# Kernel optimization log

Measured on AMD Instinct MI355X. Metric: run time of the kernel, lower is better.

Reference implementation:

```python
import jax, jax.numpy as jnp
import numpy as np
from jax import lax

EPS = 1e-5


def fps(xyz, npoint):
    # Farthest point sampling; xyz [B, N, 3] -> idx [B, npoint] (starts at point 0)
    B, N, _ = xyz.shape

    def body(carry, _):
        dist, far = carry
        c = jnp.take_along_axis(xyz, far[:, None, None], axis=1)  # [B,1,3]
        d = jnp.sum((xyz - c) ** 2, -1)                            # [B,N]
        dist = jnp.minimum(dist, d)
        nxt = jnp.argmax(dist, -1).astype(jnp.int32)
        return (dist, nxt), far

    init = (jnp.full((B, N), 1e10, xyz.dtype), jnp.zeros((B,), jnp.int32))
    _, idx = lax.scan(body, init, None, length=npoint)
    return idx.T  # [B, npoint]


def query_ball(radius, nsample, xyz, new_xyz):
    # xyz [B,N,3], new_xyz [B,S,3] -> idx [B,S,nsample]
    N = xyz.shape[1]
    sqr = jnp.sum((new_xyz[:, :, None, :] - xyz[:, None, :, :]) ** 2, -1)  # [B,S,N]
    idx = jnp.where(sqr > radius * radius, N, jnp.arange(N)[None, None, :])
    idx = jnp.sort(idx, axis=-1)[:, :, :nsample]
    # out-of-ball slots get replaced by the first in-ball index (torch repo behavior)
    return jnp.where(idx == N, idx[:, :, :1], idx)


def gather_pts(x, idx):
    # x [B,N,C], idx [B,...] -> [B,...,C]
    B = x.shape[0]
    b = jnp.arange(B).reshape((B,) + (1,) * (idx.ndim - 1))
    return x[b, idx]


def mlp_bn(x, layers):
    # x [B,S,K,C]; shared 1x1-conv MLP + training-mode BatchNorm + ReLU
    for w, g, b in layers:
        x = jnp.einsum('bskc,oc->bsko', x, w)
        mean = x.mean((0, 1, 2))
        var = x.var((0, 1, 2))  # biased, as torch BN uses for normalization
        x = jax.nn.relu((x - mean) * lax.rsqrt(var + EPS) * g + b)
    return x


def set_abstraction(xyz, points, npoint, radius, nsample, layers, group_all):
    B = xyz.shape[0]
    if group_all:
        new_xyz = jnp.zeros((B, 1, 3), xyz.dtype)
        new_points = xyz[:, None]  # [B,1,N,3] (raw xyz, no centering)
        if points is not None:
            new_points = jnp.concatenate([new_points, points[:, None]], -1)
    else:
        fidx = fps(xyz, npoint)
        new_xyz = gather_pts(xyz, fidx)                     # [B,S,3]
        idx = query_ball(radius, nsample, xyz, new_xyz)     # [B,S,K]
        grouped = gather_pts(xyz, idx) - new_xyz[:, :, None, :]
        if points is not None:
            new_points = jnp.concatenate([grouped, gather_pts(points, idx)], -1)
        else:
            new_points = grouped
    feat = mlp_bn(new_points, layers).max(2)  # max-pool over neighbors -> [B,S,C]
    return new_xyz, feat


def _forward(xyz_time, l1, l2, l3):
    B, T, N, _ = xyz_time.shape
    x = xyz_time.reshape(B * T, N, 4)
    xyz, t = x[..., :3], x[..., 3:]
    x1_xyz, x1 = set_abstraction(xyz, t, 512, 0.2, 32, l1, False)
    x2_xyz, x2 = set_abstraction(x1_xyz, x1, 128, 0.4, 64, l2, False)
    _, x3 = set_abstraction(x2_xyz, x2, None, None, None, l3, True)
    return x3.reshape(B, T, -1)


def setup_inputs() -> dict:
    key = jax.random.key(0)
    ks = jax.random.split(key, 16)
    inp = {"xyz_time": jax.random.uniform(ks[0], (2, 4, 4096, 4), jnp.float32)}
    specs = {1: [(64, 4), (64, 64), (128, 64)],
             2: [(128, 131), (128, 128), (256, 128)],
             3: [(256, 259), (512, 256), (1024, 512)]}
    i = 1
    for s, layers in specs.items():
        for j, (o, c) in enumerate(layers):
            inp[f"w{s}_{j}"] = jax.random.normal(jax.random.fold_in(ks[i], j), (o, c), jnp.float32) * 0.1
            inp[f"g{s}_{j}"] = jnp.ones((o,), jnp.float32)
            inp[f"b{s}_{j}"] = jnp.zeros((o,), jnp.float32)
        i += 1
    return inp


def reference(xyz_time, w1_0, g1_0, b1_0, w1_1, g1_1, b1_1, w1_2, g1_2, b1_2,
              w2_0, g2_0, b2_0, w2_1, g2_1, b2_1, w2_2, g2_2, b2_2,
              w3_0, g3_0, b3_0, w3_1, g3_1, b3_1, w3_2, g3_2, b3_2):
    l1 = [(w1_0, g1_0, b1_0), (w1_1, g1_1, b1_1), (w1_2, g1_2, b1_2)]
    l2 = [(w2_0, g2_0, b2_0), (w2_1, g2_1, b2_1), (w2_2, g2_2, b2_2)]
    l3 = [(w3_0, g3_0, b3_0), (w3_1, g3_1, b3_1), (w3_2, g3_2, b3_2)]
    return _forward(xyz_time, l1, l2, l3)
```

## Files before the change

kernel.cpp:

```cpp
#include <hip/hip_runtime.h>


typedef short s16x8 __attribute__((ext_vector_type(8)));
typedef float f32x4 __attribute__((ext_vector_type(4)));

__device__ __forceinline__ unsigned short f2bf_rne(float f) {
    unsigned u = __float_as_uint(f);
    u += 0x7FFFu + ((u >> 16) & 1u);
    return (unsigned short)(u >> 16);
}
__device__ __forceinline__ void f2bf_split(float v, unsigned short& hi,
                                           unsigned short& lo) {
    unsigned u = __float_as_uint(v);
    unsigned r = u + 0x7FFFu + ((u >> 16) & 1u);
    hi = (unsigned short)(r >> 16);
    float vh = __uint_as_float(r & 0xFFFF0000u);
    lo = f2bf_rne(v - vh);
}

__device__ __forceinline__ unsigned long long umax64(unsigned long long a,
                                                     unsigned long long b) {
    return a > b ? a : b;
}

__device__ __forceinline__ unsigned wred_umax63(unsigned v) {
    unsigned t;
    t = (unsigned)__builtin_amdgcn_update_dpp(0, (int)v, 0x111, 0xf, 0xf, true); if (t > v) v = t;
    t = (unsigned)__builtin_amdgcn_update_dpp(0, (int)v, 0x112, 0xf, 0xf, true); if (t > v) v = t;
    t = (unsigned)__builtin_amdgcn_update_dpp(0, (int)v, 0x114, 0xf, 0xf, true); if (t > v) v = t;
    t = (unsigned)__builtin_amdgcn_update_dpp(0, (int)v, 0x118, 0xf, 0xf, true); if (t > v) v = t;
    t = (unsigned)__builtin_amdgcn_update_dpp(0, (int)v, 0x142, 0xa, 0xf, true); if (t > v) v = t;
    t = (unsigned)__builtin_amdgcn_update_dpp(0, (int)v, 0x143, 0xc, 0xf, true); if (t > v) v = t;
    return v;
}

__device__ __forceinline__ void wave_argmax(unsigned dbits, unsigned nInv,
                                            unsigned& vmax, unsigned& iInv) {
    unsigned m = wred_umax63(dbits);
    vmax = (unsigned)__builtin_amdgcn_readlane((int)m, 63);
    unsigned cand = (dbits == vmax) ? nInv : 0u;
    unsigned im = wred_umax63(cand);
    iInv = (unsigned)__builtin_amdgcn_readlane((int)im, 63);
}

struct PWArgs {
    const float* w[9];
    unsigned off[9];
    int O[9], C[9], CP[9];
};
__device__ __forceinline__ void prep_w_dev(const PWArgs& a,
                                           unsigned short* __restrict__ wh,
                                           unsigned short* __restrict__ wl,
                                           int i) {
    int l = 0;
#pragma unroll
    for (int k = 1; k < 9; ++k) if (i >= (int)a.off[k]) l = k;
    int li = i - (int)a.off[l];
    int CP = a.CP[l];
    int o = li / CP;
    int c = li - o * CP;
    float v = (c < a.C[l]) ? a.w[l][(size_t)o * a.C[l] + c] : 0.f;
    unsigned short h, lo;
    f2bf_split(v, h, lo);
    wh[i] = h; wl[i] = lo;
}

template<int NT, int ITEMS, int STRIDE>
__global__ __launch_bounds__(NT) void fps_block(
    const float* __restrict__ pts, int npoint,
    int* __restrict__ outIdx, float* __restrict__ outXyz,
    int nFps, PWArgs pw, unsigned short* __restrict__ wh,
    unsigned short* __restrict__ wl, int wtotal)
{
    constexpr int N = NT * ITEMS;
    constexpr int NW = NT / 64;
    __shared__ float4 scoord[N];
    __shared__ unsigned long long wkey[2][NW];

    if (blockIdx.x >= nFps) {
        int i = (blockIdx.x - nFps) * NT + threadIdx.x;
        if (i < wtotal) prep_w_dev(pw, wh, wl, i);
        return;
    }

    const int b = blockIdx.x;
    const int tid = threadIdx.x;
    const int wid = tid >> 6;
    const int lane = tid & 63;
    const float* P = pts + (size_t)b * N * STRIDE;

    float px[ITEMS], py[ITEMS], pz[ITEMS], dloc[ITEMS];
#pragma unroll
    for (int w = 0; w < ITEMS; ++w) {
        int n = tid + w * NT;
        float x, y, z;
        if (STRIDE == 4) {
            float4 v = *(const float4*)(P + (size_t)n * 4);
            x = v.x; y = v.y; z = v.z;
        } else {
            x = P[(size_t)n * STRIDE + 0];
            y = P[(size_t)n * STRIDE + 1];
            z = P[(size_t)n * STRIDE + 2];
        }
        px[w] = x; py[w] = y; pz[w] = z;
        scoord[n] = make_float4(x, y, z, 0.f);
        dloc[w] = 1e10f;
    }
    __syncthreads();
    float4 c0 = scoord[0];
    float cx = c0.x, cy = c0.y, cz = c0.z;
    int far = 0;

    for (int i = 0; i < npoint; ++i) {
        if (tid == 0) {
            outIdx[(size_t)b * npoint + i] = far;
            outXyz[((size_t)b * npoint + i) * 3 + 0] = cx;
            outXyz[((size_t)b * npoint + i) * 3 + 1] = cy;
            outXyz[((size_t)b * npoint + i) * 3 + 2] = cz;
        }
        float bestV = -1.0f;
        int bestW = 0;
#pragma unroll
        for (int w = 0; w < ITEMS; ++w) {
            float dx = __fsub_rn(px[w], cx);
            float dy = __fsub_rn(py[w], cy);
            float dz = __fsub_rn(pz[w], cz);
            float d = __fadd_rn(__fadd_rn(__fmul_rn(dx, dx), __fmul_rn(dy, dy)),
                                __fmul_rn(dz, dz));
            float dd = fminf(dloc[w], d);
            dloc[w] = dd;
            if (dd > bestV) { bestV = dd; bestW = w; }
        }
        int bestN = tid + bestW * NT;
        unsigned vmax, iInv;
        wave_argmax(__float_as_uint(bestV), 0xFFFFFFFFu ^ (unsigned)bestN,
                    vmax, iInv);
        const int par = i & 1;
        if (lane == 0)
            wkey[par][wid] = ((unsigned long long)vmax << 32) | iInv;
        __syncthreads();
        unsigned long long kb = wkey[par][0];
#pragma unroll
        for (int w2 = 1; w2 < NW; ++w2) kb = umax64(kb, wkey[par][w2]);
        far = (int)(0xFFFFFFFFu ^ (unsigned)kb);
        float4 cc = scoord[far];
        cx = cc.x; cy = cc.y; cz = cc.z;
    }
}

__device__ void fps_wave_dev(const float* __restrict__ pts, int npoint,
                             int* __restrict__ outIdx, float* __restrict__ outXyz,
                             int b, float4* scoord)
{
    constexpr int ITEMS = 8;
    constexpr int STRIDE = 3;
    constexpr int N = 64 * ITEMS;
    const int tid = threadIdx.x;
    const float* P = pts + (size_t)b * N * STRIDE;

    float px[ITEMS], py[ITEMS], pz[ITEMS], dloc[ITEMS];
#pragma unroll
    for (int w = 0; w < ITEMS; ++w) {
        int n = tid + w * 64;
        float x = P[(size_t)n * STRIDE + 0];
        float y = P[(size_t)n * STRIDE + 1];
        float z = P[(size_t)n * STRIDE + 2];
        px[w] = x; py[w] = y; pz[w] = z;
        scoord[n] = make_float4(x, y, z, 0.f);
        dloc[w] = 1e10f;
    }
    __threadfence_block();
    float4 c0 = scoord[0];
    float cx = c0.x, cy = c0.y, cz = c0.z;
    int far = 0;

    for (int i = 0; i < npoint; ++i) {
        if (tid == 0) {
            outIdx[(size_t)b * npoint + i] = far;
            outXyz[((size_t)b * npoint + i) * 3 + 0] = cx;
            outXyz[((size_t)b * npoint + i) * 3 + 1] = cy;
            outXyz[((size_t)b * npoint + i) * 3 + 2] = cz;
        }
        float bestV = -1.0f;
        int bestW = 0;
#pragma unroll
        for (int w = 0; w < ITEMS; ++w) {
            float dx = __fsub_rn(px[w], cx);
            float dy = __fsub_rn(py[w], cy);
            float dz = __fsub_rn(pz[w], cz);
            float d = __fadd_rn(__fadd_rn(__fmul_rn(dx, dx), __fmul_rn(dy, dy)),
                                __fmul_rn(dz, dz));
            float dd = fminf(dloc[w], d);
            dloc[w] = dd;
            if (dd > bestV) { bestV = dd; bestW = w; }
        }
        int bestN = tid + bestW * 64;
        unsigned vmax, iInv;
        wave_argmax(__float_as_uint(bestV), 0xFFFFFFFFu ^ (unsigned)bestN,
                    vmax, iInv);
        far = (int)(0xFFFFFFFFu ^ iInv);
        float4 cc = scoord[far];
        cx = cc.x; cy = cc.y; cz = cc.z;
    }
}

__global__ __launch_bounds__(256) void qb_group1(
    const float* __restrict__ xyz ,
    const float* __restrict__ ctr ,
    float* __restrict__ out )
{
    int gw = (blockIdx.x * 256 + threadIdx.x) >> 6;
    int lane = threadIdx.x & 63;
    if (gw >= 4096) return;
    int b = gw >> 9;
    const float* P = xyz + (size_t)b * 4096 * 4;
    float cx = ctr[(size_t)gw * 3 + 0];
    float cy = ctr[(size_t)gw * 3 + 1];
    float cz = ctr[(size_t)gw * 3 + 2];
    float* out0 = out + (size_t)gw * 32 * 8;
    int cnt = 0;
    float f0x = 0.f, f0y = 0.f, f0z = 0.f, f0t = 0.f;
    bool haveFirst = false;
    for (int base = 0; base < 4096 && cnt < 32; base += 64) {
        int n = base + lane;
        float4 p = *(const float4*)(P + (size_t)n * 4);
        float ex = __fsub_rn(p.x, cx);
        float ey = __fsub_rn(p.y, cy);
        float ez = __fsub_rn(p.z, cz);
        float d = __fadd_rn(__fadd_rn(__fmul_rn(ex, ex), __fmul_rn(ey, ey)),
                            __fmul_rn(ez, ez));
        bool inb = !(d > 0.04f);
        unsigned long long mask = __ballot(inb);
        if (mask) {
            if (!haveFirst) {
                int fl = (int)__builtin_ctzll(mask);
                f0x = __shfl(ex, fl); f0y = __shfl(ey, fl);
                f0z = __shfl(ez, fl); f0t = __shfl(p.w, fl);
                haveFirst = true;
            }
            if (inb) {
                int pos = cnt + __builtin_popcountll(mask & ((1ull << lane) - 1ull));
                if (pos < 32) {
                    float* o = out0 + (size_t)pos * 8;
                    *(float4*)o = make_float4(ex, ey, ez, p.w);
                    *(float4*)(o + 4) = make_float4(0.f, 0.f, 0.f, 0.f);
                }
            }
            cnt += (int)__builtin_popcountll(mask);
        }
    }
    if (cnt > 32) cnt = 32;
    for (int p2 = cnt + lane; p2 < 32; p2 += 64) {
        float* o = out0 + (size_t)p2 * 8;
        *(float4*)o = make_float4(f0x, f0y, f0z, f0t);
        *(float4*)(o + 4) = make_float4(0.f, 0.f, 0.f, 0.f);
    }
}

__global__ __launch_bounds__(256) void query_ball_kernel(
    const float* __restrict__ xyz, int stride, int N,
    const float* __restrict__ centers, int nCenters, int S,
    float r2, int nsample, int* __restrict__ outIdx)
{
    int gw = (blockIdx.x * 256 + threadIdx.x) >> 6;
    int lane = threadIdx.x & 63;
    if (gw >= nCenters) return;
    int b = gw / S;
    const float* P = xyz + (size_t)b * N * stride;
    float cx = centers[(size_t)gw * 3 + 0];
    float cy = centers[(size_t)gw * 3 + 1];
    float cz = centers[(size_t)gw * 3 + 2];
    int* out = outIdx + (size_t)gw * nsample;
    int cnt = 0;
    int firstIdx = 0;
    bool haveFirst = false;
    for (int base = 0; base < N && cnt < nsample; base += 64) {
        int n = base + lane;
        bool inb = false;
        if (n < N) {
            float dx = __fsub_rn(cx, P[(size_t)n * stride + 0]);
            float dy = __fsub_rn(cy, P[(size_t)n * stride + 1]);
            float dz = __fsub_rn(cz, P[(size_t)n * stride + 2]);
            float d = __fadd_rn(__fadd_rn(__fmul_rn(dx, dx), __fmul_rn(dy, dy)),
                                __fmul_rn(dz, dz));
            inb = !(d > r2);
        }
        unsigned long long mask = __ballot(inb);
        if (mask) {
            if (!haveFirst) { firstIdx = base + __builtin_ctzll(mask); haveFirst = true; }
            if (inb) {
                int pos = cnt + __builtin_popcountll(mask & ((1ull << lane) - 1ull));
                if (pos < nsample) out[pos] = n;
            }
            cnt += (int)__builtin_popcountll(mask);
        }
    }
    if (cnt > nsample) cnt = nsample;
    for (int p = cnt + lane; p < nsample; p += 64) out[p] = firstIdx;
}

__global__ __launch_bounds__(256) void group2_kernel(
    const float* __restrict__ xyz, const float* __restrict__ feat,
    const int* __restrict__ qb, const float* __restrict__ ctr,
    float* __restrict__ out)
{
    int i = blockIdx.x * 256 + threadIdx.x;
    if (i >= 65536 * 136) return;
    int sk = i / 136;
    int c = i - sk * 136;
    int b = sk / (128 * 64);
    int bs = sk / 64;
    int idx = qb[sk];
    idx = (idx < 0) ? 0 : (idx > 511 ? 511 : idx);
    float v = 0.f;
    if (c < 3)        v = __fsub_rn(xyz[((size_t)b * 512 + idx) * 3 + c], ctr[(size_t)bs * 3 + c]);
    else if (c < 131) v = feat[((size_t)b * 512 + idx) * 128 + (c - 3)];
    out[i] = v;
}

__global__ __launch_bounds__(256) void group3_kernel(
    const float* __restrict__ ctr2, const float* __restrict__ feat2,
    float* __restrict__ out)
{
    int i = blockIdx.x * 256 + threadIdx.x;
    if (i >= 1024 * 264) return;
    int sk = i / 264;
    int c = i - sk * 264;
    float v = 0.f;
    if (c < 3)        v = ctr2[(size_t)sk * 3 + c];
    else if (c < 259) v = feat2[(size_t)sk * 256 + (c - 3)];
    out[i] = v;
}

__global__ __launch_bounds__(256) void gemm_fused(
    const float* __restrict__ X,
    const float* __restrict__ scale, const float* __restrict__ shift,
    int applyAct,
    const unsigned short* __restrict__ Bh, const unsigned short* __restrict__ Bl,
    float* __restrict__ Y, double* __restrict__ part,
    int M, int AC, int CPW, int O, int YBmain,
    const float* __restrict__ fpsPts, int fpsNpoint,
    int* __restrict__ fpsIdx, float* __restrict__ fpsXyz)
{
    constexpr int PITCH = 40;
    __shared__ __align__(16) unsigned short sAh[128 * PITCH];
    __shared__ __align__(16) unsigned short sAl[128 * PITCH];
    __shared__ __align__(16) unsigned short sBh[128 * PITCH];
    __shared__ __align__(16) unsigned short sBl[128 * PITCH];
    __shared__ float sred[2048];

    if ((int)blockIdx.x >= YBmain) {
        if (threadIdx.x < 64 && fpsPts != nullptr)
            fps_wave_dev(fpsPts, fpsNpoint, fpsIdx, fpsXyz,
                         (int)blockIdx.x - YBmain, (float4*)sAh);
        return;
    }

    const int tid = threadIdx.x;
    const int lane = tid & 63;
    const int wid = tid >> 6;
    const int col15 = lane & 15;
    const int quad = lane >> 4;
    const int wm = (wid >> 1) * 64;
    const int wo = (wid & 1) * 64;
    const int m0 = blockIdx.x * 128;
    const int o0 = blockIdx.y * 128;
    const int YB = YBmain;
    const int lr = tid >> 2;
    const int lc = (tid & 3) * 8;

    f32x4 acc[4][4];
#pragma unroll
    for (int mt = 0; mt < 4; ++mt)
#pragma unroll
        for (int ot = 0; ot < 4; ++ot)
            acc[mt][ot] = {0.f, 0.f, 0.f, 0.f};

    for (int k0 = 0; k0 < CPW; k0 += 32) {
#pragma unroll
        for (int it = 0; it < 2; ++it) {
            int r = lr + it * 64;
            int c = k0 + lc;
            unsigned short h[8], l[8];
            if (c + 8 <= AC) {
                const float* xr = X + (size_t)(m0 + r) * AC + c;
                float4 v0 = *(const float4*)xr;
                float4 v1 = *(const float4*)(xr + 4);
                float vv[8] = {v0.x, v0.y, v0.z, v0.w, v1.x, v1.y, v1.z, v1.w};
#pragma unroll
                for (int j = 0; j < 8; ++j) {
                    float v = vv[j];
                    if (applyAct) v = fmaxf(v * scale[c + j] + shift[c + j], 0.f);
                    f2bf_split(v, h[j], l[j]);
                }
            } else {
#pragma unroll
                for (int j = 0; j < 8; ++j) { h[j] = 0; l[j] = 0; }
            }
            *(ushort4*)&sAh[r * PITCH + lc] = make_ushort4(h[0], h[1], h[2], h[3]);
            *(ushort4*)&sAh[r * PITCH + lc + 4] = make_ushort4(h[4], h[5], h[6], h[7]);
            *(ushort4*)&sAl[r * PITCH + lc] = make_ushort4(l[0], l[1], l[2], l[3]);
            *(ushort4*)&sAl[r * PITCH + lc + 4] = make_ushort4(l[4], l[5], l[6], l[7]);
        }
#pragma unroll
        for (int it = 0; it < 2; ++it) {
            int r = lr + it * 64;
            int c = k0 + lc;
            int o = o0 + r;
            uint4 vh = {0, 0, 0, 0}, vl = {0, 0, 0, 0};
            if (o < O && c < CPW) {
                size_t goff = (size_t)o * CPW + c;
                vh = *(const uint4*)(Bh + goff);
                vl = *(const uint4*)(Bl + goff);
            }
            *(uint4*)&sBh[r * PITCH + lc] = vh;
            *(uint4*)&sBl[r * PITCH + lc] = vl;
        }
        __syncthreads();
        s16x8 ah[4], al[4], bh[4], bl[4];
#pragma unroll
        for (int mt = 0; mt < 4; ++mt) {
            int rowoff = (wm + mt * 16 + col15) * PITCH + quad * 8;
            ah[mt] = *(const s16x8*)&sAh[rowoff];
            al[mt] = *(const s16x8*)&sAl[rowoff];
        }
#pragma unroll
        for (int ot = 0; ot < 4; ++ot) {
            int rowoff = (wo + ot * 16 + col15) * PITCH + quad * 8;
            bh[ot] = *(const s16x8*)&sBh[rowoff];
            bl[ot] = *(const s16x8*)&sBl[rowoff];
        }
#pragma unroll
        for (int mt = 0; mt < 4; ++mt)
#pragma unroll
            for (int ot = 0; ot < 4; ++ot) {
                acc[mt][ot] = __builtin_amdgcn_mfma_f32_16x16x32_bf16(
                    ah[mt], bl[ot], acc[mt][ot], 0, 0, 0);
                acc[mt][ot] = __builtin_amdgcn_mfma_f32_16x16x32_bf16(
                    al[mt], bh[ot], acc[mt][ot], 0, 0, 0);
                acc[mt][ot] = __builtin_amdgcn_mfma_f32_16x16x32_bf16(
                    ah[mt], bh[ot], acc[mt][ot], 0, 0, 0);
            }
        __syncthreads();
    }
#pragma unroll
    for (int mt = 0; mt < 4; ++mt)
#pragma unroll
        for (int ot = 0; ot < 4; ++ot) {
            int og = o0 + wo + ot * 16 + col15;
            if (og < O) {
#pragma unroll
                for (int r = 0; r < 4; ++r) {
                    int mg = m0 + wm + mt * 16 + quad * 4 + r;
                    Y[(size_t)mg * O + og] = acc[mt][ot][r];
                }
            }
        }
#pragma unroll
    for (int ot = 0; ot < 4; ++ot) {
        float s = 0.f, s2 = 0.f;
#pragma unroll
        for (int mt = 0; mt < 4; ++mt)
#pragma unroll
            for (int r = 0; r < 4; ++r) {
                float v = acc[mt][ot][r];
                s += v;
                s2 += v * v;
            }
        int slot = ((wid * 4 + quad) * 16 + col15) * 4 + ot;
        sred[slot * 2] = s;
        sred[slot * 2 + 1] = s2;
    }
    __syncthreads();
    if (tid < 128) {
        int col = tid;
        int o = o0 + col;
        if (o < O) {
            int cb = col >> 6;
            int ot = (col & 63) >> 4;
            int c15 = col & 15;
            double S = 0.0, S2 = 0.0;
#pragma unroll
            for (int wp = 0; wp < 2; ++wp) {
                int wd = cb + wp * 2;
#pragma unroll
                for (int q = 0; q < 4; ++q) {
                    int slot = ((wd * 4 + q) * 16 + c15) * 4 + ot;
                    S += (double)sred[slot * 2];
                    S2 += (double)sred[slot * 2 + 1];
                }
            }
            part[(size_t)o * YB + blockIdx.x] = S;
            part[(size_t)O * YB + (size_t)o * YB + blockIdx.x] = S2;
        }
    }
}

__global__ __launch_bounds__(256) void finalize_bn(
    const double* __restrict__ part, const float* __restrict__ g,
    const float* __restrict__ bb, float* __restrict__ scale,
    float* __restrict__ shift, int O, int YB, double invM)
{
    int o = blockIdx.x;
    int tid = threadIdx.x;
    double s = 0.0, s2 = 0.0;
    for (int yb = tid; yb < YB; yb += 256) {
        s  += part[(size_t)o * YB + yb];
        s2 += part[(size_t)O * YB + (size_t)o * YB + yb];
    }
    __shared__ double sd[512];
    sd[tid] = s;
    sd[256 + tid] = s2;
    __syncthreads();
#pragma unroll
    for (int st = 128; st > 0; st >>= 1) {
        if (tid < st) {
            sd[tid] += sd[tid + st];
            sd[256 + tid] += sd[256 + tid + st];
        }
        __syncthreads();
    }
    if (tid == 0) {
        double mean = sd[0] * invM;
        double var = sd[256] * invM - mean * mean;
        float varf = (float)var;
        if (varf < 0.f) varf = 0.f;
        float sc = g[o] * rsqrtf(varf + 1e-5f);
        scale[o] = sc;
        shift[o] = bb[o] - (float)mean * sc;
    }
}

__global__ __launch_bounds__(256) void bn_relu_max(
    const float* __restrict__ Y, const float* __restrict__ scale,
    const float* __restrict__ shift, float* __restrict__ out,
    int Stot, int K, int O)
{
    int idx = blockIdx.x * 256 + threadIdx.x;
    if (idx >= Stot * O) return;
    int s = idx / O;
    int o = idx - s * O;
    const float* base = Y + (size_t)s * K * O + o;
    float sc = scale[o], sh = shift[o];
    float mx = 0.f;
    for (int k = 0; k < K; ++k) {
        float v = base[(size_t)k * O] * sc + sh;
        v = fmaxf(v, 0.f);
        mx = fmaxf(mx, v);
    }
    out[idx] = mx;
}

extern "C" void kernel_launch(void* const* d_in, const int* in_sizes, int n_in,
                              void* d_out, int out_size, void* d_ws, size_t ws_size,
                              hipStream_t stream)
{
    const float* xin = (const float*)d_in[0];
    const float* w[9]; const float* g[9]; const float* bb[9];
    for (int i = 0; i < 9; ++i) {
        w[i]  = (const float*)d_in[1 + 3 * i];
        g[i]  = (const float*)d_in[2 + 3 * i];
        bb[i] = (const float*)d_in[3 + 3 * i];
    }

    char* base = (char*)d_ws;
    size_t off = 0;
    auto alloc = [&](size_t bytes) -> void* {
        void* p = base + off;
        off = (off + bytes + 255) & ~(size_t)255;
        return p;
    };
    const int OC[9][3] = {{64,4,8},{64,64,64},{128,64,64},
                          {128,131,136},{128,128,128},{256,128,128},
                          {256,259,264},{512,256,256},{1024,512,512}};
    size_t woff[10]; woff[0] = 0;
    for (int i = 0; i < 9; ++i) woff[i + 1] = woff[i] + (size_t)OC[i][0] * OC[i][2];

    int*    fps1   = (int*)alloc((size_t)4096 * 4);
    int*    fps2   = (int*)alloc((size_t)1024 * 4);
    int*    qb2    = (int*)alloc((size_t)65536 * 4);
    float*  nx1    = (float*)alloc((size_t)12288 * 4);
    float*  nx2    = (float*)alloc((size_t)3072 * 4);
    float*  feat1  = (float*)alloc((size_t)524288 * 4);
    float*  feat2  = (float*)alloc((size_t)262144 * 4);
    double* part   = (double*)alloc((size_t)262144 * 8);
    float*  scales = (float*)alloc((size_t)9 * 1024 * 4);
    float*  shifts = (float*)alloc((size_t)9 * 1024 * 4);
    unsigned short* WH = (unsigned short*)alloc(woff[9] * 2);
    unsigned short* WL = (unsigned short*)alloc(woff[9] * 2);
    const size_t zeroBytes = off;
    float*  XG = (float*)alloc((size_t)65536 * 136 * 4);
    float*  A  = (float*)alloc((size_t)16777216 * 4);
    if (off > ws_size) return;

    hipMemsetAsync(d_ws, 0, zeroBytes, stream);

    PWArgs pwa;
    for (int i = 0; i < 9; ++i) {
        pwa.w[i] = w[i]; pwa.off[i] = (unsigned)woff[i];
        pwa.O[i] = OC[i][0]; pwa.C[i] = OC[i][1]; pwa.CP[i] = OC[i][2];
    }
    const int nPrep = (int)((woff[9] + 255) / 256);

    fps_block<256, 16, 4><<<8 + nPrep, 256, 0, stream>>>(
        xin, 512, fps1, nx1, 8, pwa, WH, WL, (int)woff[9]);
    qb_group1<<<(4096 * 64) / 256, 256, 0, stream>>>(xin, nx1, XG);

    gemm_fused<<<dim3(1024, 1), 256, 0, stream>>>(XG, nullptr, nullptr, 0, WH + woff[0], WL + woff[0], A, part, 131072, 8, 8, 64, 1024, nullptr, 0, nullptr, nullptr);
    finalize_bn<<<64, 256, 0, stream>>>(part, g[0], bb[0], scales + 0 * 1024, shifts + 0 * 1024, 64, 1024, 1.0 / 131072.0);
    gemm_fused<<<dim3(1024, 1), 256, 0, stream>>>(A, scales + 0 * 1024, shifts + 0 * 1024, 1, WH + woff[1], WL + woff[1], XG, part, 131072, 64, 64, 64, 1024, nullptr, 0, nullptr, nullptr);
    finalize_bn<<<64, 256, 0, stream>>>(part, g[1], bb[1], scales + 1 * 1024, shifts + 1 * 1024, 64, 1024, 1.0 / 131072.0);
    gemm_fused<<<dim3(1024 + 8, 1), 256, 0, stream>>>(XG, scales + 1 * 1024, shifts + 1 * 1024, 1, WH + woff[2], WL + woff[2], A, part, 131072, 64, 64, 128, 1024, nx1, 128, fps2, nx2);
    finalize_bn<<<128, 256, 0, stream>>>(part, g[2], bb[2], scales + 2 * 1024, shifts + 2 * 1024, 128, 1024, 1.0 / 131072.0);
    bn_relu_max<<<(4096 * 128) / 256, 256, 0, stream>>>(A, scales + 2 * 1024, shifts + 2 * 1024, feat1, 4096, 32, 128);

    query_ball_kernel<<<(8 * 128 * 64) / 256, 256, 0, stream>>>(
        nx1, 3, 512, nx2, 8 * 128, 128, 0.16f, 64, qb2);
    group2_kernel<<<(65536 * 136) / 256, 256, 0, stream>>>(nx1, feat1, qb2, nx2, XG);

    gemm_fused<<<dim3(512, 1), 256, 0, stream>>>(XG, nullptr, nullptr, 0, WH + woff[3], WL + woff[3], A, part, 65536, 136, 136, 128, 512, nullptr, 0, nullptr, nullptr);
    finalize_bn<<<128, 256, 0, stream>>>(part, g[3], bb[3], scales + 3 * 1024, shifts + 3 * 1024, 128, 512, 1.0 / 65536.0);
    gemm_fused<<<dim3(512, 1), 256, 0, stream>>>(A, scales + 3 * 1024, shifts + 3 * 1024, 1, WH + woff[4], WL + woff[4], XG, part, 65536, 128, 128, 128, 512, nullptr, 0, nullptr, nullptr);
    finalize_bn<<<128, 256, 0, stream>>>(part, g[4], bb[4], scales + 4 * 1024, shifts + 4 * 1024, 128, 512, 1.0 / 65536.0);
    gemm_fused<<<dim3(512, 2), 256, 0, stream>>>(XG, scales + 4 * 1024, shifts + 4 * 1024, 1, WH + woff[5], WL + woff[5], A, part, 65536, 128, 128, 256, 512, nullptr, 0, nullptr, nullptr);
    finalize_bn<<<256, 256, 0, stream>>>(part, g[5], bb[5], scales + 5 * 1024, shifts + 5 * 1024, 256, 512, 1.0 / 65536.0);
    bn_relu_max<<<(1024 * 256) / 256, 256, 0, stream>>>(A, scales + 5 * 1024, shifts + 5 * 1024, feat2, 1024, 64, 256);

    group3_kernel<<<(1024 * 264) / 256, 256, 0, stream>>>(nx2, feat2, XG);

    gemm_fused<<<dim3(8, 2), 256, 0, stream>>>(XG, nullptr, nullptr, 0, WH + woff[6], WL + woff[6], A, part, 1024, 264, 264, 256, 8, nullptr, 0, nullptr, nullptr);
    finalize_bn<<<256, 256, 0, stream>>>(part, g[6], bb[6], scales + 6 * 1024, shifts + 6 * 1024, 256, 8, 1.0 / 1024.0);
    gemm_fused<<<dim3(8, 4), 256, 0, stream>>>(A, scales + 6 * 1024, shifts + 6 * 1024, 1, WH + woff[7], WL + woff[7], XG, part, 1024, 256, 256, 512, 8, nullptr, 0, nullptr, nullptr);
    finalize_bn<<<512, 256, 0, stream>>>(part, g[7], bb[7], scales + 7 * 1024, shifts + 7 * 1024, 512, 8, 1.0 / 1024.0);
    gemm_fused<<<dim3(8, 8), 256, 0, stream>>>(XG, scales + 7 * 1024, shifts + 7 * 1024, 1, WH + woff[8], WL + woff[8], A, part, 1024, 512, 512, 1024, 8, nullptr, 0, nullptr, nullptr);
    finalize_bn<<<1024, 256, 0, stream>>>(part, g[8], bb[8], scales + 8 * 1024, shifts + 8 * 1024, 1024, 8, 1.0 / 1024.0);
    bn_relu_max<<<(8 * 1024) / 256, 256, 0, stream>>>(A, scales + 8 * 1024, shifts + 8 * 1024, (float*)d_out, 8, 128, 1024);
}
```

Measured before the change: 826.1 us.

## Fuse SA1 MLP layers into one cooperative kernel with grid-synced BatchNorm

Replaces the three SA1 GEMM launches, their finalize_bn launches and the max-pool with a single cooperative kernel of 512 blocks. Each block keeps two 128-row tiles of activations in registers and shared memory across all three layers, and uses grid.sync to reduce BatchNorm statistics. This avoids writing and re-reading the large intermediate activations to global memory and removes several launches. The second-level FPS moves from the third GEMM into the qb_group1 launch. If the cooperative launch fails, the old path runs instead. The risks are register pressure from six accumulator tile sets and the cost of the grid-wide barriers.

```diff
diff --git a/kernel.cpp b/kernel.cpp
--- a/kernel.cpp
+++ b/kernel.cpp
@@ -1,4 +1,7 @@
 #include <hip/hip_runtime.h>
+#include <hip/hip_cooperative_groups.h>
+
+namespace cg = cooperative_groups;
 
 
 typedef short s16x8 __attribute__((ext_vector_type(8)));
@@ -207,8 +210,17 @@
 __global__ __launch_bounds__(256) void qb_group1(
     const float* __restrict__ xyz ,
     const float* __restrict__ ctr ,
-    float* __restrict__ out )
-{
+    float* __restrict__ out ,
+    int nQb, const float* __restrict__ fpsPts,
+    int* __restrict__ fpsIdx, float* __restrict__ fpsXyz)
+{
+    __shared__ float4 scoord[512];
+    if ((int)blockIdx.x >= nQb) {
+        if (threadIdx.x < 64)
+            fps_wave_dev(fpsPts, 128, fpsIdx, fpsXyz,
+                         (int)blockIdx.x - nQb, scoord);
+        return;
+    }
     int gw = (blockIdx.x * 256 + threadIdx.x) >> 6;
     int lane = threadIdx.x & 63;
     if (gw >= 4096) return;
@@ -332,15 +344,286 @@
     out[i] = v;
 }
 
+#define SA1_PITCH 72
+
+template<int NCHUNK, int CPWv, int Ov>
+__device__ __forceinline__ void sa1_gemm(f32x4 (&acc)[4][4],
+    const unsigned short* sAh, const unsigned short* sAl,
+    const unsigned short* __restrict__ Bh, const unsigned short* __restrict__ Bl,
+    int wm, int wo, int col15, int quad)
+{
+#pragma unroll
+    for (int mt = 0; mt < 4; ++mt)
+#pragma unroll
+        for (int ot = 0; ot < 4; ++ot) acc[mt][ot] = {0.f, 0.f, 0.f, 0.f};
+#pragma unroll
+    for (int ch = 0; ch < NCHUNK; ++ch) {
+        const int k0 = ch * 32;
+        s16x8 ah[4], al[4], bh[4], bl[4];
+#pragma unroll
+        for (int mt = 0; mt < 4; ++mt) {
+            int ro = (wm + mt * 16 + col15) * SA1_PITCH + k0 + quad * 8;
+            ah[mt] = *(const s16x8*)&sAh[ro];
+            al[mt] = *(const s16x8*)&sAl[ro];
+        }
+#pragma unroll
+        for (int ot = 0; ot < 4; ++ot) {
+            int orow = wo + ot * 16 + col15;
+            if (orow < Ov && k0 + quad * 8 < CPWv) {
+                size_t go = (size_t)orow * CPWv + k0 + quad * 8;
+                bh[ot] = *(const s16x8*)(Bh + go);
+                bl[ot] = *(const s16x8*)(Bl + go);
+            } else {
+                bh[ot] = {0, 0, 0, 0, 0, 0, 0, 0};
+                bl[ot] = {0, 0, 0, 0, 0, 0, 0, 0};
+            }
+        }
+#pragma unroll
+        for (int mt = 0; mt < 4; ++mt)
+#pragma unroll
+            for (int ot = 0; ot < 4; ++ot) {
+                acc[mt][ot] = __builtin_amdgcn_mfma_f32_16x16x32_bf16(
+                    ah[mt], bl[ot], acc[mt][ot], 0, 0, 0);
+                acc[mt][ot] = __builtin_amdgcn_mfma_f32_16x16x32_bf16(
+                    al[mt], bh[ot], acc[mt][ot], 0, 0, 0);
+                acc[mt][ot] = __builtin_amdgcn_mfma_f32_16x16x32_bf16(
+                    ah[mt], bh[ot], acc[mt][ot], 0, 0, 0);
+            }
+    }
+}
+
+__device__ __forceinline__ void sa1_stage_x(
+    unsigned short* sAh, unsigned short* sAl,
+    const float* __restrict__ XG, int m0, int lr, int lc)
+{
+    __syncthreads();
+#pragma unroll
+    for (int it = 0; it < 2; ++it) {
+        int r = lr + it * 64;
+        unsigned short h[8], l[8];
+        if (lc == 0) {
+            const float* xr = XG + (size_t)(m0 + r) * 8;
+            float4 v0 = *(const float4*)xr;
+            float4 v1 = *(const float4*)(xr + 4);
+            float vv[8] = {v0.x, v0.y, v0.z, v0.w, v1.x, v1.y, v1.z, v1.w};
+#pragma unroll
+            for (int j = 0; j < 8; ++j) f2bf_split(vv[j], h[j], l[j]);
+        } else {
+#pragma unroll
+            for (int j = 0; j < 8; ++j) { h[j] = 0; l[j] = 0; }
+        }
+        *(ushort4*)&sAh[r * SA1_PITCH + lc]     = make_ushort4(h[0], h[1], h[2], h[3]);
+        *(ushort4*)&sAh[r * SA1_PITCH + lc + 4] = make_ushort4(h[4], h[5], h[6], h[7]);
+        *(ushort4*)&sAl[r * SA1_PITCH + lc]     = make_ushort4(l[0], l[1], l[2], l[3]);
+        *(ushort4*)&sAl[r * SA1_PITCH + lc + 4] = make_ushort4(l[4], l[5], l[6], l[7]);
+    }
+    __syncthreads();
+}
+
+__device__ __forceinline__ void sa1_stage_act(
+    unsigned short* sAh, unsigned short* sAl, const f32x4 (&acc)[4][4],
+    const float* __restrict__ sc, const float* __restrict__ sh,
+    int wm, int wo, int col15, int quad)
+{
+    __syncthreads();
+    if (wo == 0) {
+#pragma unroll
+        for (int ot = 0; ot < 4; ++ot) {
+            int c = ot * 16 + col15;
+            float s = sc[c], b = sh[c];
+#pragma unroll
+            for (int mt = 0; mt < 4; ++mt)
+#pragma unroll
+                for (int r = 0; r < 4; ++r) {
+                    int m = wm + mt * 16 + quad * 4 + r;
+                    float v = fmaxf(acc[mt][ot][r] * s + b, 0.f);
+                    unsigned short hh, ll;
+                    f2bf_split(v, hh, ll);
+                    sAh[m * SA1_PITCH + c] = hh;
+                    sAl[m * SA1_PITCH + c] = ll;
+                }
+        }
+    }
+    __syncthreads();
+}
+
+__device__ __forceinline__ void sa1_stats(
+    const f32x4 (&a0)[4][4], const f32x4 (&a1)[4][4], float* sred,
+    double* __restrict__ part, int Ov, int bx, int tid, int wid,
+    int quad, int col15)
+{
+#pragma unroll
+    for (int ot = 0; ot < 4; ++ot) {
+        float s = 0.f, s2 = 0.f;
+#pragma unroll
+        for (int mt = 0; mt < 4; ++mt)
+#pragma unroll
+            for (int r = 0; r < 4; ++r) { float v = a0[mt][ot][r]; s += v; s2 += v * v; }
+#pragma unroll
+        for (int mt = 0; mt < 4; ++mt)
+#pragma unroll
+            for (int r = 0; r < 4; ++r) { float v = a1[mt][ot][r]; s += v; s2 += v * v; }
+        int slot = ((wid * 4 + quad) * 16 + col15) * 4 + ot;
+        sred[slot * 2] = s;
+        sred[slot * 2 + 1] = s2;
+    }
+    __syncthreads();
+    if (tid < 128) {
+        int col = tid, o = col;
+        if (o < Ov) {
+            int cb = col >> 6, ot = (col & 63) >> 4, c15 = col & 15;
+            double S = 0.0, S2 = 0.0;
+#pragma unroll
+            for (int wp = 0; wp < 2; ++wp) {
+                int wd = cb + wp * 2;
+#pragma unroll
+                for (int q = 0; q < 4; ++q) {
+                    int slot = ((wd * 4 + q) * 16 + c15) * 4 + ot;
+                    S += (double)sred[slot * 2];
+                    S2 += (double)sred[slot * 2 + 1];
+                }
+            }
+            part[(size_t)o * 512 + bx] = S;
+            part[(size_t)Ov * 512 + (size_t)o * 512 + bx] = S2;
+        }
+    }
+}
+
+__device__ __forceinline__ void sa1_finalize(
+    const double* __restrict__ part, int Ov, const float* __restrict__ gl,
+    const float* __restrict__ bbl, float* __restrict__ scl,
+    float* __restrict__ shl, double* sd, int bx, int tid)
+{
+    if (bx < Ov) {
+        double s  = part[(size_t)bx * 512 + tid] + part[(size_t)bx * 512 + 256 + tid];
+        size_t b2 = (size_t)Ov * 512 + (size_t)bx * 512;
+        double s2 = part[b2 + tid] + part[b2 + 256 + tid];
+        sd[tid] = s;
+        sd[256 + tid] = s2;
+        __syncthreads();
+#pragma unroll
+        for (int st = 128; st > 0; st >>= 1) {
+            if (tid < st) {
+                sd[tid] += sd[tid + st];
+                sd[256 + tid] += sd[256 + tid + st];
+            }
+            __syncthreads();
+        }
+        if (tid == 0) {
+            double mean = sd[0] * (1.0 / 131072.0);
+            double var = sd[256] * (1.0 / 131072.0) - mean * mean;
+            float varf = (float)var;
+            if (varf < 0.f) varf = 0.f;
+            float sc = gl[bx] * rsqrtf(varf + 1e-5f);
+            scl[bx] = sc;
+            shl[bx] = bbl[bx] - (float)mean * sc;
+        }
+    }
+}
+
+__device__ __forceinline__ void sa1_epi(
+    const f32x4 (&acc)[4][4], const float* __restrict__ sc2,
+    const float* __restrict__ sh2, float* __restrict__ feat1,
+    int tile, int wm, int wo, int col15, int quad)
+{
+#pragma unroll
+    for (int ot = 0; ot < 4; ++ot) {
+        int og = wo + ot * 16 + col15;
+        float s = sc2[og], b = sh2[og];
+        float m01 = 0.f, m23 = 0.f;
+#pragma unroll
+        for (int r = 0; r < 4; ++r) {
+            m01 = fmaxf(m01, fmaxf(acc[0][ot][r] * s + b, 0.f));
+            m01 = fmaxf(m01, fmaxf(acc[1][ot][r] * s + b, 0.f));
+            m23 = fmaxf(m23, fmaxf(acc[2][ot][r] * s + b, 0.f));
+            m23 = fmaxf(m23, fmaxf(acc[3][ot][r] * s + b, 0.f));
+        }
+        m01 = fmaxf(m01, __shfl_xor(m01, 16));
+        m01 = fmaxf(m01, __shfl_xor(m01, 32));
+        m23 = fmaxf(m23, __shfl_xor(m23, 16));
+        m23 = fmaxf(m23, __shfl_xor(m23, 32));
+        if (quad == 0) {
+            int cb = tile * 4 + (wm >> 5);
+            feat1[(size_t)cb * 128 + og] = m01;
+            feat1[(size_t)(cb + 1) * 128 + og] = m23;
+        }
+    }
+}
+
+__global__ __launch_bounds__(256, 2) void sa1_fused(
+    const float* __restrict__ XG,
+    const unsigned short* __restrict__ WH0, const unsigned short* __restrict__ WL0,
+    const unsigned short* __restrict__ WH1, const unsigned short* __restrict__ WL1,
+    const unsigned short* __restrict__ WH2, const unsigned short* __restrict__ WL2,
+    const float* __restrict__ g0, const float* __restrict__ b0,
+    const float* __restrict__ g1, const float* __restrict__ b1,
+    const float* __restrict__ g2, const float* __restrict__ b2,
+    double* __restrict__ part, float* __restrict__ scales,
+    float* __restrict__ shifts, float* __restrict__ feat1)
+{
+    __shared__ __align__(16) unsigned short sAh[128 * SA1_PITCH];
+    __shared__ __align__(16) unsigned short sAl[128 * SA1_PITCH];
+    __shared__ __align__(16) float sred[2048];
+    cg::grid_group grid = cg::this_grid();
+
+    const int tid = threadIdx.x;
+    const int lane = tid & 63;
+    const int wid = tid >> 6;
+    const int col15 = lane & 15;
+    const int quad = lane >> 4;
+    const int wm = (wid >> 1) * 64;
+    const int wo = (wid & 1) * 64;
+    const int bx = blockIdx.x;
+    const int lr = tid >> 2;
+    const int lc = (tid & 3) * 8;
+    const int m0t0 = bx * 128, m0t1 = (bx + 512) * 128;
+
+    f32x4 a0t0[4][4], a0t1[4][4], a1t0[4][4], a1t1[4][4], a2t0[4][4], a2t1[4][4];
+
+    sa1_stage_x(sAh, sAl, XG, m0t0, lr, lc);
+    sa1_gemm<1, 8, 64>(a0t0, sAh, sAl, WH0, WL0, wm, wo, col15, quad);
+    sa1_stage_x(sAh, sAl, XG, m0t1, lr, lc);
+    sa1_gemm<1, 8, 64>(a0t1, sAh, sAl, WH0, WL0, wm, wo, col15, quad);
+    sa1_stats(a0t0, a0t1, sred, part, 64, bx, tid, wid, quad, col15);
+    __threadfence();
+    grid.sync();
+    sa1_finalize(part, 64, g0, b0, scales + 0, shifts + 0, (double*)sred, bx, tid);
+    __threadfence();
+    grid.sync();
+
+    sa1_stage_act(sAh, sAl, a0t0, scales + 0, shifts + 0, wm, wo, col15, quad);
+    sa1_gemm<2, 64, 64>(a1t0, sAh, sAl, WH1, WL1, wm, wo, col15, quad);
+    sa1_stage_act(sAh, sAl, a0t1, scales + 0, shifts + 0, wm, wo, col15, quad);
+    sa1_gemm<2, 64, 64>(a1t1, sAh, sAl, WH1, WL1, wm, wo, col15, quad);
+    sa1_stats(a1t0, a1t1, sred, part, 64, bx, tid, wid, quad, col15);
+    __threadfence();
+    grid.sync();
+    sa1_finalize(part, 64, g1, b1, scales + 1024, shifts + 1024, (double*)sred, bx, tid);
+    __threadfence();
+    grid.sync();
+
+    sa1_stage_act(sAh, sAl, a1t0, scales + 1024, shifts + 1024, wm, wo, col15, quad);
+    sa1_gemm<2, 64, 128>(a2t0, sAh, sAl, WH2, WL2, wm, wo, col15, quad);
+    sa1_stage_act(sAh, sAl, a1t1, scales + 1024, shifts + 1024, wm, wo, col15, quad);
+    sa1_gemm<2, 64, 128>(a2t1, sAh, sAl, WH2, WL2, wm, wo, col15, quad);
+    sa1_stats(a2t0, a2t1, sred, part, 128, bx, tid, wid, quad, col15);
+    __threadfence();
+    grid.sync();
+    sa1_finalize(part, 128, g2, b2, scales + 2048, shifts + 2048, (double*)sred, bx, tid);
+    __threadfence();
+    grid.sync();
+
+    sa1_epi(a2t0, scales + 2048, shifts + 2048, feat1, bx, wm, wo, col15, quad);
+    sa1_epi(a2t1, scales + 2048, shifts + 2048, feat1, bx + 512, wm, wo, col15, quad);
+}
+
 __global__ __launch_bounds__(256) void gemm_fused(
     const float* __restrict__ X,
     const float* __restrict__ scale, const float* __restrict__ shift,
     int applyAct,
     const unsigned short* __restrict__ Bh, const unsigned short* __restrict__ Bl,
     float* __restrict__ Y, double* __restrict__ part,
-    int M, int AC, int CPW, int O, int YBmain,
-    const float* __restrict__ fpsPts, int fpsNpoint,
-    int* __restrict__ fpsIdx, float* __restrict__ fpsXyz)
+    int M, int AC, int CPW, int O, int YBmain)
 {
     constexpr int PITCH = 40;
     __shared__ __align__(16) unsigned short sAh[128 * PITCH];
@@ -348,13 +631,6 @@
     __shared__ __align__(16) unsigned short sBh[128 * PITCH];
     __shared__ __align__(16) unsigned short sBl[128 * PITCH];
     __shared__ float sred[2048];
-
-    if ((int)blockIdx.x >= YBmain) {
-        if (threadIdx.x < 64 && fpsPts != nullptr)
-            fps_wave_dev(fpsPts, fpsNpoint, fpsIdx, fpsXyz,
-                         (int)blockIdx.x - YBmain, (float4*)sAh);
-        return;
-    }
 
     const int tid = threadIdx.x;
     const int lane = tid & 63;
@@ -604,35 +880,56 @@
 
     fps_block<256, 16, 4><<<8 + nPrep, 256, 0, stream>>>(
         xin, 512, fps1, nx1, 8, pwa, WH, WL, (int)woff[9]);
-    qb_group1<<<(4096 * 64) / 256, 256, 0, stream>>>(xin, nx1, XG);
-
-    gemm_fused<<<dim3(1024, 1), 256, 0, stream>>>(XG, nullptr, nullptr, 0, WH + woff[0], WL + woff[0], A, part, 131072, 8, 8, 64, 1024, nullptr, 0, nullptr, nullptr);
-    finalize_bn<<<64, 256, 0, stream>>>(part, g[0], bb[0], scales + 0 * 1024, shifts + 0 * 1024, 64, 1024, 1.0 / 131072.0);
-    gemm_fused<<<dim3(1024, 1), 256, 0, stream>>>(A, scales + 0 * 1024, shifts + 0 * 1024, 1, WH + woff[1], WL + woff[1], XG, part, 131072, 64, 64, 64, 1024, nullptr, 0, nullptr, nullptr);
-    finalize_bn<<<64, 256, 0, stream>>>(part, g[1], bb[1], scales + 1 * 1024, shifts + 1 * 1024, 64, 1024, 1.0 / 131072.0);
-    gemm_fused<<<dim3(1024 + 8, 1), 256, 0, stream>>>(XG, scales + 1 * 1024, shifts + 1 * 1024, 1, WH + woff[2], WL + woff[2], A, part, 131072, 64, 64, 128, 1024, nx1, 128, fps2, nx2);
-    finalize_bn<<<128, 256, 0, stream>>>(part, g[2], bb[2], scales + 2 * 1024, shifts + 2 * 1024, 128, 1024, 1.0 / 131072.0);
-    bn_relu_max<<<(4096 * 128) / 256, 256, 0, stream>>>(A, scales + 2 * 1024, shifts + 2 * 1024, feat1, 4096, 32, 128);
+    qb_group1<<<1024 + 8, 256, 0, stream>>>(xin, nx1, XG, 1024, nx1, fps2, nx2);
+
+    {
+        const float* aXG = XG;
+        const unsigned short* wh0 = WH + woff[0]; const unsigned short* wl0 = WL + woff[0];
+        const unsigned short* wh1 = WH + woff[1]; const unsigned short* wl1 = WL + woff[1];
+        const unsigned short* wh2 = WH + woff[2]; const unsigned short* wl2 = WL + woff[2];
+        const float* ag0 = g[0]; const float* ab0 = bb[0];
+        const float* ag1 = g[1]; const float* ab1 = bb[1];
+        const float* ag2 = g[2]; const float* ab2 = bb[2];
+        double* apart = part; float* ascales = scales; float* ashifts = shifts;
+        float* afeat1 = feat1;
+        void* kargs[] = {
+            (void*)&aXG, (void*)&wh0, (void*)&wl0, (void*)&wh1, (void*)&wl1,
+            (void*)&wh2, (void*)&wl2, (void*)&ag0, (void*)&ab0, (void*)&ag1,
+            (void*)&ab1, (void*)&ag2, (void*)&ab2, (void*)&apart,
+            (void*)&ascales, (void*)&ashifts, (void*)&afeat1
+        };
+        hipError_t ce = hipLaunchCooperativeKernel(
+            (const void*)sa1_fused, dim3(512), dim3(256), kargs, 0, stream);
+        if (ce != hipSuccess) {
+            gemm_fused<<<dim3(1024, 1), 256, 0, stream>>>(XG, nullptr, nullptr, 0, WH + woff[0], WL + woff[0], A, part, 131072, 8, 8, 64, 1024);
+            finalize_bn<<<64, 256, 0, stream>>>(part, g[0], bb[0], scales + 0 * 1024, shifts + 0 * 1024, 64, 1024, 1.0 / 131072.0);
+            gemm_fused<<<dim3(1024, 1), 256, 0, stream>>>(A, scales + 0 * 1024, shifts + 0 * 1024, 1, WH + woff[1], WL + woff[1], XG, part, 131072, 64, 64, 64, 1024);
+            finalize_bn<<<64, 256, 0, stream>>>(part, g[1], bb[1], scales + 1 * 1024, shifts + 1 * 1024, 64, 1024, 1.0 / 131072.0);
+            gemm_fused<<<dim3(1024, 1), 256, 0, stream>>>(XG, scales + 1 * 1024, shifts + 1 * 1024, 1, WH + woff[2], WL + woff[2], A, part, 131072, 64, 64, 128, 1024);
+            finalize_bn<<<128, 256, 0, stream>>>(part, g[2], bb[2], scales + 2 * 1024, shifts + 2 * 1024, 128, 1024, 1.0 / 131072.0);
+            bn_relu_max<<<(4096 * 128) / 256, 256, 0, stream>>>(A, scales + 2 * 1024, shifts + 2 * 1024, feat1, 4096, 32, 128);
+        }
+    }
 
     query_ball_kernel<<<(8 * 128 * 64) / 256, 256, 0, stream>>>(
         nx1, 3, 512, nx2, 8 * 128, 128, 0.16f, 64, qb2);
     group2_kernel<<<(65536 * 136) / 256, 256, 0, stream>>>(nx1, feat1, qb2, nx2, XG);
 
-    gemm_fused<<<dim3(512, 1), 256, 0, stream>>>(XG, nullptr, nullptr, 0, WH + woff[3], WL + woff[3], A, part, 65536, 136, 136, 128, 512, nullptr, 0, nullptr, nullptr);
+    gemm_fused<<<dim3(512, 1), 256, 0, stream>>>(XG, nullptr, nullptr, 0, WH + woff[3], WL + woff[3], A, part, 65536, 136, 136, 128, 512);
     finalize_bn<<<128, 256, 0, stream>>>(part, g[3], bb[3], scales + 3 * 1024, shifts + 3 * 1024, 128, 512, 1.0 / 65536.0);
-    gemm_fused<<<dim3(512, 1), 256, 0, stream>>>(A, scales + 3 * 1024, shifts + 3 * 1024, 1, WH + woff[4], WL + woff[4], XG, part, 65536, 128, 128, 128, 512, nullptr, 0, nullptr, nullptr);
+    gemm_fused<<<dim3(512, 1), 256, 0, stream>>>(A, scales + 3 * 1024, shifts + 3 * 1024, 1, WH + woff[4], WL + woff[4], XG, part, 65536, 128, 128, 128, 512);
     finalize_bn<<<128, 256, 0, stream>>>(part, g[4], bb[4], scales + 4 * 1024, shifts + 4 * 1024, 128, 512, 1.0 / 65536.0);
-    gemm_fused<<<dim3(512, 2), 256, 0, stream>>>(XG, scales + 4 * 1024, shifts + 4 * 1024, 1, WH + woff[5], WL + woff[5], A, part, 65536, 128, 128, 256, 512, nullptr, 0, nullptr, nullptr);
+    gemm_fused<<<dim3(512, 2), 256, 0, stream>>>(XG, scales + 4 * 1024, shifts + 4 * 1024, 1, WH + woff[5], WL + woff[5], A, part, 65536, 128, 128, 256, 512);
     finalize_bn<<<256, 256, 0, stream>>>(part, g[5], bb[5], scales + 5 * 1024, shifts + 5 * 1024, 256, 512, 1.0 / 65536.0);
     bn_relu_max<<<(1024 * 256) / 256, 256, 0, stream>>>(A, scales + 5 * 1024, shifts + 5 * 1024, feat2, 1024, 64, 256);
 
     group3_kernel<<<(1024 * 264) / 256, 256, 0, stream>>>(nx2, feat2, XG);
 
-    gemm_fused<<<dim3(8, 2), 256, 0, stream>>>(XG, nullptr, nullptr, 0, WH + woff[6], WL + woff[6], A, part, 1024, 264, 264, 256, 8, nullptr, 0, nullptr, nullptr);
+    gemm_fused<<<dim3(8, 2), 256, 0, stream>>>(XG, nullptr, nullptr, 0, WH + woff[6], WL + woff[6], A, part, 1024, 264, 264, 256, 8);
     finalize_bn<<<256, 256, 0, stream>>>(part, g[6], bb[6], scales + 6 * 1024, shifts + 6 * 1024, 256, 8, 1.0 / 1024.0);
-    gemm_fused<<<dim3(8, 4), 256, 0, stream>>>(A, scales + 6 * 1024, shifts + 6 * 1024, 1, WH + woff[7], WL + woff[7], XG, part, 1024, 256, 256, 512, 8, nullptr, 0, nullptr, nullptr);
+    gemm_fused<<<dim3(8, 4), 256, 0, stream>>>(A, scales + 6 * 1024, shifts + 6 * 1024, 1, WH + woff[7], WL + woff[7], XG, part, 1024, 256, 256, 512, 8);
     finalize_bn<<<512, 256, 0, stream>>>(part, g[7], bb[7], scales + 7 * 1024, shifts + 7 * 1024, 512, 8, 1.0 / 1024.0);
-    gemm_fused<<<dim3(8, 8), 256, 0, stream>>>(XG, scales + 7 * 1024, shifts + 7 * 1024, 1, WH + woff[8], WL + woff[8], A, part, 1024, 512, 512, 1024, 8, nullptr, 0, nullptr, nullptr);
+    gemm_fused<<<dim3(8, 8), 256, 0, stream>>>(XG, scales + 7 * 1024, shifts + 7 * 1024, 1, WH + woff[8], WL + woff[8], A, part, 1024, 512, 512, 1024, 8);
     finalize_bn<<<1024, 256, 0, stream>>>(part, g[8], bb[8], scales + 8 * 1024, shifts + 8 * 1024, 1024, 8, 1.0 / 1024.0);
     bn_relu_max<<<(8 * 1024) / 256, 256, 0, stream>>>(A, scales + 8 * 1024, shifts + 8 * 1024, (float*)d_out, 8, 128, 1024);
 }
```

Result: slower. 1.384 ms (+67.6%).
